# Performance work log

Hardware: AMD Instinct MI355X
Metric: run time of the kernel (lower is better)

Reference implementation:

```python
import jax, jax.numpy as jnp
import numpy as np

ALPHA = 0.5
MOM = 0.9            # momentum m in the recurrence
ACTIVATION = "tanh"
NUM_LAYERS = 2
CACHE = 32           # GROUP size
NK = 4               # n_kernel_feats
B, N, E = 4, 4096, 128


def _act(T):
    if ACTIVATION == "leaky-relu":
        return jax.nn.leaky_relu(T)
    elif ACTIVATION == "tanh":
        return jnp.tanh(T)
    return T


def _group_indices(N, cache, stage):
    # vectorized group_pos_to_index_v2 over all (group_nr, pos_in_group)
    m = N // cache
    o = np.arange(cache)
    s = 0 if stage == 0 else (1 << (stage - 1)) % m
    g = np.arange(m)[:, None]
    block = (g + o[None, :] * s) % m
    return jnp.asarray(block * cache + o[None, :])  # [m, cache], a permutation of 0..N-1


def _ncn_layer(X, Xa, W, stage):
    B, N, E = X.shape
    ce = E // NK
    m = N // CACHE
    idx = _group_indices(N, CACHE, stage)           # [m, cache]
    Wi = W[:E].reshape(NK, ce)
    Wj = W[E:].reshape(NK, ce)
    # gather groups: [B, m, NK, cache, ce]
    xg = jnp.moveaxis(X.reshape(B, N, NK, ce)[:, idx], 3, 2)
    xag = jnp.moveaxis(Xa.reshape(B, N, NK, ce)[:, idx], 3, 2)

    def step(carry, j):
        xi, xa = carry                               # [B, m, NK, cache, ce]
        xj = jnp.take(xi, j, axis=3)                 # [B, m, NK, ce]  (row start_j)
        sim = (jnp.einsum('bgnke,ne->bgnk', xi, Wi)
               + jnp.einsum('bgne,ne->bgn', xj, Wj)[..., None])   # [B, m, NK, cache]
        T = ALPHA * xi + (1.0 - ALPHA) * sim[..., None] * xj[:, :, :, None, :]
        F = _act(T)
        ya = MOM * xa + (1.0 - MOM) * F
        yi = MOM * xi + (1.0 - MOM) * ya
        return (yi, ya), None

    (yi, ya), _ = jax.lax.scan(step, (xg, xag), jnp.arange(CACHE))

    # scatter back; idx is a permutation so .set reproduces the += into zeros
    def scatter(v):
        v = jnp.moveaxis(v, 2, 3).reshape(B, m * CACHE, E)
        return jnp.zeros((B, N, E), v.dtype).at[:, idx.reshape(-1)].set(v)

    return scatter(yi), scatter(ya)


def setup_inputs() -> dict:
    key = jax.random.key(0)
    k1, k2, k3 = jax.random.split(key, 3)
    x = jax.random.normal(k1, (B, N, E), jnp.float32)
    xa = jax.random.normal(k2, (B, N, E), jnp.float32)
    W = jax.random.normal(k3, (NUM_LAYERS, 2 * E), jnp.float32)
    return {"x": x, "xa": xa, "W": W}


def reference(x, xa, W):
    for l in range(NUM_LAYERS):
        x, xa = _ncn_layer(x, xa, W[l], l)
    return x, xa
```

## Files before the change

kernel.cpp:

```cpp
#include <hip/hip_runtime.h>


namespace {
constexpr int kB = 4;
constexpr int kN = 4096;
constexpr int kE = 128;
constexpr int kCE = 32;
constexpr int kH  = 16;
constexpr int kQ  = kH / 2;
constexpr int kCache = 32;
constexpr int kM = kN / kCache;

typedef __attribute__((ext_vector_type(2))) float f32x2;

__device__ __forceinline__ f32x2 pk_fma(f32x2 a, f32x2 b, f32x2 c) {
    return __builtin_elementwise_fma(a, b, c);
}
}

__global__ void ncn_layer_kernel(
    const float* __restrict__ x_in, const float* __restrict__ xa_in,
    const float* __restrict__ Wl,
    float* __restrict__ x_out, float* __restrict__ xa_out,
    int s)
{
    const int blk = blockIdx.x;
    const int n   = blk & 3;
    const int g   = (blk >> 2) & (kM - 1);
    const int b   = blk >> 9;
    const int t   = threadIdx.x;
    const int o   = t & 31;
    const int h   = t >> 5;

    const int r = (((g + o * s) & (kM - 1)) << 5) + o;
    const size_t base = ((size_t)(b * kN + r)) * kE + n * kCE + h * kH;

    constexpr float L1 = 1.4426950408889634f;

    f32x2 xi[kQ], xa[kQ], wi[kQ], wj[kQ];

    {
        const float4* xi4 = reinterpret_cast<const float4*>(x_in + base);
        const float4* xa4 = reinterpret_cast<const float4*>(xa_in + base);
        const float4* wi4 = reinterpret_cast<const float4*>(Wl + n * kCE + h * kH);
        const float4* wj4 = reinterpret_cast<const float4*>(Wl + kE + n * kCE + h * kH);
#pragma unroll
        for (int q = 0; q < kQ / 2; ++q) {
            float4 v = xi4[q];
            xi[2 * q + 0] = f32x2{v.x, v.y}; xi[2 * q + 1] = f32x2{v.z, v.w};
            float4 a = xa4[q];
            xa[2 * q + 0] = f32x2{a.x, a.y}; xa[2 * q + 1] = f32x2{a.z, a.w};
            float4 u = wi4[q];
            wi[2 * q + 0] = f32x2{u.x * L1, u.y * L1};
            wi[2 * q + 1] = f32x2{u.z * L1, u.w * L1};
            float4 w = wj4[q];
            wj[2 * q + 0] = f32x2{w.x * L1, w.y * L1};
            wj[2 * q + 1] = f32x2{w.z * L1, w.w * L1};
        }
    }

    const int srcbase = (t & 32) * 4;

#pragma unroll 2
    for (int j = 0; j < kCache; ++j) {
        const int srcaddr = srcbase + j * 4;

        f32x2 a01 = xi[0] * wi[0];
        f32x2 a23 = xi[1] * wi[1];
        f32x2 b01 = xi[0] * wj[0];
        f32x2 b23 = xi[1] * wj[1];
#pragma unroll
        for (int q = 2; q < kQ; q += 2) {
            a01 = pk_fma(xi[q + 0], wi[q + 0], a01);
            a23 = pk_fma(xi[q + 1], wi[q + 1], a23);
            b01 = pk_fma(xi[q + 0], wj[q + 0], b01);
            b23 = pk_fma(xi[q + 1], wj[q + 1], b23);
        }
        f32x2 av = a01 + a23;
        f32x2 bv = b01 + b23;
        float part = av.x + av.y;
        float pj   = bv.x + bv.y;

        float di_o = __shfl_xor(part, 32, 64);
        float dj0  = __int_as_float(
            __builtin_amdgcn_ds_bpermute(j * 4, __float_as_int(pj)));
        float dj1  = __int_as_float(
            __builtin_amdgcn_ds_bpermute(128 + j * 4, __float_as_int(pj)));

        f32x2 xj[kQ];
#pragma unroll
        for (int q = 0; q < kQ; ++q) {
            xj[q].x = __int_as_float(
                __builtin_amdgcn_ds_bpermute(srcaddr, __float_as_int(xi[q].x)));
            xj[q].y = __int_as_float(
                __builtin_amdgcn_ds_bpermute(srcaddr, __float_as_int(xi[q].y)));
        }

        const float sim = (part + di_o) + (dj0 + dj1);
        const f32x2 sv  = {sim, sim};
        const f32x2 l12 = {L1, L1};
        const f32x2 one = {1.0f, 1.0f};
        const f32x2 m02 = {-0.2f, -0.2f};
        const f32x2 c9  = {0.9f, 0.9f};
        const f32x2 c01 = {0.1f, 0.1f};

#pragma unroll
        for (int q = 0; q < kQ; ++q) {
            f32x2 arg = pk_fma(xj[q], sv, xi[q] * l12);
            f32x2 t2;
            t2.x = __builtin_amdgcn_exp2f(arg.x);
            t2.y = __builtin_amdgcn_exp2f(arg.y);
            f32x2 den = t2 + one;
            f32x2 rc;
            rc.x = __builtin_amdgcn_rcpf(den.x);
            rc.y = __builtin_amdgcn_rcpf(den.y);
            xa[q] = pk_fma(m02, rc, pk_fma(c9, xa[q], c01));
            xi[q] = pk_fma(c01, xa[q], xi[q] * c9);
        }
    }

    {
        float4* xo4 = reinterpret_cast<float4*>(x_out + base);
        float4* ao4 = reinterpret_cast<float4*>(xa_out + base);
#pragma unroll
        for (int q = 0; q < kQ / 2; ++q) {
            float4 v;
            v.x = xi[2 * q + 0].x; v.y = xi[2 * q + 0].y;
            v.z = xi[2 * q + 1].x; v.w = xi[2 * q + 1].y;
            xo4[q] = v;
            float4 a;
            a.x = xa[2 * q + 0].x; a.y = xa[2 * q + 0].y;
            a.z = xa[2 * q + 1].x; a.w = xa[2 * q + 1].y;
            ao4[q] = a;
        }
    }
}

extern "C" void kernel_launch(void* const* d_in, const int* in_sizes, int n_in,
                              void* d_out, int out_size, void* d_ws, size_t ws_size,
                              hipStream_t stream) {
    const float* x  = (const float*)d_in[0];
    const float* xa = (const float*)d_in[1];
    const float* W  = (const float*)d_in[2];

    const size_t plane = (size_t)kB * kN * kE;

    float* x_mid  = (float*)d_ws;
    float* xa_mid = x_mid + plane;

    float* x_out  = (float*)d_out;
    float* xa_out = x_out + plane;

    const dim3 grid(kB * kM * 4);
    const dim3 block(64);

    ncn_layer_kernel<<<grid, block, 0, stream>>>(x, xa, W, x_mid, xa_mid, 0);
    ncn_layer_kernel<<<grid, block, 0, stream>>>(x_mid, xa_mid, W + 2 * kE,
                                                 x_out, xa_out, 1);
}
```

Before: 123.5 us.

## Broadcast pivot row via shared memory instead of per-element bpermutes

Replaces the sixteen ds_bpermute broadcasts of row j per step with a shared-memory row buffer. The owning lane writes its updated row after each step and all lanes read it as float4 loads. Because every lane now holds xj, the sim dot products merge into a single reduction with one cross-half shuffle. The cost is a __syncthreads per iteration plus divergent writes, and launch bounds are added along with a larger unroll.

Result: no change. 124.1 us (+0.5%).

```diff
diff --git a/kernel.cpp b/kernel.cpp
--- a/kernel.cpp
+++ b/kernel.cpp
@@ -18,7 +18,7 @@
 }
 }
 
-__global__ void ncn_layer_kernel(
+__global__ void __launch_bounds__(64, 2) ncn_layer_kernel(
     const float* __restrict__ x_in, const float* __restrict__ xa_in,
     const float* __restrict__ Wl,
     float* __restrict__ x_out, float* __restrict__ xa_out,
@@ -59,44 +59,48 @@
         }
     }
 
-    const int srcbase = (t & 32) * 4;
+    __shared__ float rowbuf[kCE];
 
-#pragma unroll 2
+    if (o == 0) {
+        float4* w4 = reinterpret_cast<float4*>(&rowbuf[h * kH]);
+#pragma unroll
+        for (int q = 0; q < kQ / 2; ++q) {
+            float4 v;
+            v.x = xi[2 * q + 0].x; v.y = xi[2 * q + 0].y;
+            v.z = xi[2 * q + 1].x; v.w = xi[2 * q + 1].y;
+            w4[q] = v;
+        }
+    }
+    __syncthreads();
+
+#pragma unroll 4
     for (int j = 0; j < kCache; ++j) {
-        const int srcaddr = srcbase + j * 4;
+        f32x2 xj[kQ];
+        {
+            const float4* r4 = reinterpret_cast<const float4*>(&rowbuf[h * kH]);
+#pragma unroll
+            for (int q = 0; q < kQ / 2; ++q) {
+                float4 v = r4[q];
+                xj[2 * q + 0] = f32x2{v.x, v.y};
+                xj[2 * q + 1] = f32x2{v.z, v.w};
+            }
+        }
 
         f32x2 a01 = xi[0] * wi[0];
         f32x2 a23 = xi[1] * wi[1];
-        f32x2 b01 = xi[0] * wj[0];
-        f32x2 b23 = xi[1] * wj[1];
+        f32x2 b01 = xj[0] * wj[0];
+        f32x2 b23 = xj[1] * wj[1];
 #pragma unroll
         for (int q = 2; q < kQ; q += 2) {
             a01 = pk_fma(xi[q + 0], wi[q + 0], a01);
             a23 = pk_fma(xi[q + 1], wi[q + 1], a23);
-            b01 = pk_fma(xi[q + 0], wj[q + 0], b01);
-            b23 = pk_fma(xi[q + 1], wj[q + 1], b23);
+            b01 = pk_fma(xj[q + 0], wj[q + 0], b01);
+            b23 = pk_fma(xj[q + 1], wj[q + 1], b23);
         }
-        f32x2 av = a01 + a23;
-        f32x2 bv = b01 + b23;
-        float part = av.x + av.y;
-        float pj   = bv.x + bv.y;
+        f32x2 uv = (a01 + a23) + (b01 + b23);
+        float u  = uv.x + uv.y;
 
-        float di_o = __shfl_xor(part, 32, 64);
-        float dj0  = __int_as_float(
-            __builtin_amdgcn_ds_bpermute(j * 4, __float_as_int(pj)));
-        float dj1  = __int_as_float(
-            __builtin_amdgcn_ds_bpermute(128 + j * 4, __float_as_int(pj)));
-
-        f32x2 xj[kQ];
-#pragma unroll
-        for (int q = 0; q < kQ; ++q) {
-            xj[q].x = __int_as_float(
-                __builtin_amdgcn_ds_bpermute(srcaddr, __float_as_int(xi[q].x)));
-            xj[q].y = __int_as_float(
-                __builtin_amdgcn_ds_bpermute(srcaddr, __float_as_int(xi[q].y)));
-        }
-
-        const float sim = (part + di_o) + (dj0 + dj1);
+        const float sim = u + __shfl_xor(u, 32, 64);
         const f32x2 sv  = {sim, sim};
         const f32x2 l12 = {L1, L1};
         const f32x2 one = {1.0f, 1.0f};
@@ -117,6 +121,18 @@
             xa[q] = pk_fma(m02, rc, pk_fma(c9, xa[q], c01));
             xi[q] = pk_fma(c01, xa[q], xi[q] * c9);
         }
+
+        if (o == ((j + 1) & 31)) {
+            float4* w4 = reinterpret_cast<float4*>(&rowbuf[h * kH]);
+#pragma unroll
+            for (int q = 0; q < kQ / 2; ++q) {
+                float4 v;
+                v.x = xi[2 * q + 0].x; v.y = xi[2 * q + 0].y;
+                v.z = xi[2 * q + 1].x; v.w = xi[2 * q + 1].y;
+                w4[q] = v;
+            }
+        }
+        __syncthreads();
     }
 
     {
```
